# Kernel optimization log

Hardware: AMD Instinct MI355X
Metric: run time of the kernel (lower is better)

## Reference

```python
import jax, jax.numpy as jnp
import numpy as np
from jax import lax

NUM_CLUSTER = 128
N_ITERS = 10


def setup_inputs() -> dict:
    key = jax.random.key(0)
    feat_g = jax.random.normal(key, (131072, 256), dtype=jnp.float32)
    return {"feat_g": feat_g}


def _sq_dists(x, c):
    x2 = jnp.sum(x * x, axis=1, keepdims=True)            # [N,1]
    c2 = jnp.sum(c * c, axis=1)                           # [K]
    return x2 - 2.0 * (x @ c.T) + c2[None, :]


def _kmeans_fit(x, k, iters):
    n = x.shape[0]
    init_c = x[:k]  # deterministic init: first k points
    ones = jnp.ones((n,), dtype=x.dtype)

    def step(c, _):
        assign = jnp.argmin(_sq_dists(x, c), axis=1)                 # [N]
        sums = jax.ops.segment_sum(x, assign, num_segments=k)       # [K,d]
        counts = jax.ops.segment_sum(ones, assign, num_segments=k)  # [K]
        new_c = sums / jnp.maximum(counts, 1.0)[:, None]
        new_c = jnp.where(counts[:, None] > 0, new_c, c)  # keep empty clusters
        return new_c, None

    c, _ = lax.scan(step, init_c, None, length=iters)
    return c


def reference(feat_g):
    # view(batch, -1, dim) then view(-1, dim) is an identity reshape for the math
    x = lax.stop_gradient(feat_g)  # original detaches feat_gc before fit/predict
    c = _kmeans_fit(x, NUM_CLUSTER, N_ITERS)
    preds = jnp.argmin(_sq_dists(x, c), axis=1)  # [N] int labels
    return preds
```

## Files before the change

### kernel.cpp

```cpp
#include <hip/hip_runtime.h>

#define NPTS 131072
#define DIM 256
#define NK 128
#define NITER 10
#define SEG 16

typedef _Float16 half8 __attribute__((ext_vector_type(8)));
typedef _Float16 half4v __attribute__((ext_vector_type(4)));
typedef float f32x4 __attribute__((ext_vector_type(4)));

#define RSCALE 4096.0f
#define RINV 2.44140625e-4f

__global__ void x2_kernel(const float* __restrict__ x, float* __restrict__ x2) {
  int tid = threadIdx.x;
  int p = blockIdx.x * 16 + (tid >> 4);
  int part = tid & 15;
  const float4* xr = (const float4*)(x + (size_t)p * DIM);
  float s = 0.f;
#pragma unroll
  for (int j = 0; j < 4; ++j) {
    float4 v = xr[part * 4 + j];
    s += v.x * v.x;
    s += v.y * v.y;
    s += v.z * v.z;
    s += v.w * v.w;
  }
#pragma unroll
  for (int m = 8; m >= 1; m >>= 1) s += __shfl_xor(s, m, 16);
  if (part == 0) x2[p] = s;
}

__global__ void c2_kernel(const float* __restrict__ c, float* __restrict__ c2) {
  int k = blockIdx.x, lane = threadIdx.x;
  float4 v = ((const float4*)(c + (size_t)k * DIM))[lane];
  float s = v.x * v.x + v.y * v.y + v.z * v.z + v.w * v.w;
#pragma unroll
  for (int m = 32; m >= 1; m >>= 1) s += __shfl_xor(s, m, 64);
  if (lane == 0) c2[k] = s;
}

__global__ void convert_x_kernel(const float* __restrict__ x, _Float16* __restrict__ x1,
                                 _Float16* __restrict__ x2s) {
  int i = blockIdx.x * 256 + threadIdx.x;
  float4 v = ((const float4*)x)[i];
  float f[4] = {v.x, v.y, v.z, v.w};
  half4v h, l;
#pragma unroll
  for (int j = 0; j < 4; ++j) {
    _Float16 hi = (_Float16)f[j];
    float r = f[j] - (float)hi;
    h[j] = hi;
    l[j] = (_Float16)(r * RSCALE);
  }
  ((half4v*)x1)[i] = h;
  ((half4v*)x2s)[i] = l;
}

__global__ void convert_c_kernel(const float* __restrict__ c, _Float16* __restrict__ ct) {
  int i = blockIdx.x * 256 + threadIdx.x;
  int k = i >> 6;
  int d4 = i & 63;
  float4 v = ((const float4*)c)[i];
  float f[4] = {v.x, v.y, v.z, v.w};
  half4v h, l;
#pragma unroll
  for (int j = 0; j < 4; ++j) {
    _Float16 hi = (_Float16)f[j];
    float r = f[j] - (float)hi;
    h[j] = hi;
    l[j] = (_Float16)(r * RSCALE);
  }
  int ch = d4 >> 3;
  int idx4 = ch * 2048 + k * 8 + (d4 & 7);
  ((half4v*)ct)[idx4] = h;
  ((half4v*)ct)[idx4 + 1024] = l;
}

__global__ __launch_bounds__(256, 2) void assign_mfma_kernel(
    const _Float16* __restrict__ x1, const _Float16* __restrict__ x2s,
    const _Float16* __restrict__ ct, const float* __restrict__ x2,
    const float* __restrict__ c2, int* __restrict__ out) {
  __shared__ __align__(16) _Float16 cbuf[2][8192];

  int tid = threadIdx.x;
  int lane = tid & 63;
  int w = tid >> 6;
  int lcol = lane & 15;
  int lgrp = lane >> 4;
  int row0 = blockIdx.x * 128 + w * 32;

  const _Float16* xa = x1 + (size_t)(row0 + lcol) * DIM + lgrp * 8;
  const _Float16* xb = x2s + (size_t)(row0 + lcol) * DIM + lgrp * 8;
  const half8* ctv = (const half8*)ct;

  f32x4 acc1[2][8], acc2[2][8];
#pragma unroll
  for (int rt = 0; rt < 2; ++rt)
#pragma unroll
    for (int c8 = 0; c8 < 8; ++c8) {
      acc1[rt][c8] = f32x4{0.f, 0.f, 0.f, 0.f};
      acc2[rt][c8] = f32x4{0.f, 0.f, 0.f, 0.f};
    }

  half8 A1[2], A2[2], nA1[2], nA2[2], sreg[4];

#pragma unroll
  for (int r = 0; r < 4; ++r) sreg[r] = ctv[r * 256 + tid];
#pragma unroll
  for (int rt = 0; rt < 2; ++rt) {
    A1[rt] = *(const half8*)(xa + rt * 16 * DIM);
    A2[rt] = *(const half8*)(xb + rt * 16 * DIM);
  }
#pragma unroll
  for (int r = 0; r < 4; ++r) ((half8*)cbuf[0])[r * 256 + tid] = sreg[r];
  __syncthreads();

#pragma unroll
  for (int ck = 0; ck < 8; ++ck) {
    const int cb = ck & 1;
    if (ck < 7) {
#pragma unroll
      for (int r = 0; r < 4; ++r) sreg[r] = ctv[(ck + 1) * 1024 + r * 256 + tid];
#pragma unroll
      for (int rt = 0; rt < 2; ++rt) {
        nA1[rt] = *(const half8*)(xa + rt * 16 * DIM + (ck + 1) * 32);
        nA2[rt] = *(const half8*)(xb + rt * 16 * DIM + (ck + 1) * 32);
      }
    }
#pragma unroll
    for (int c8 = 0; c8 < 8; ++c8) {
      int bidx = (c8 * 16 + lcol) * 32 + lgrp * 8;
      half8 b1 = *(const half8*)&cbuf[cb][bidx];
      half8 b2 = *(const half8*)&cbuf[cb][4096 + bidx];
#pragma unroll
      for (int rt = 0; rt < 2; ++rt) {
        acc1[rt][c8] = __builtin_amdgcn_mfma_f32_16x16x32_f16(A1[rt], b1, acc1[rt][c8], 0, 0, 0);
        acc2[rt][c8] = __builtin_amdgcn_mfma_f32_16x16x32_f16(A1[rt], b2, acc2[rt][c8], 0, 0, 0);
        acc2[rt][c8] = __builtin_amdgcn_mfma_f32_16x16x32_f16(A2[rt], b1, acc2[rt][c8], 0, 0, 0);
      }
    }
    if (ck < 7) {
#pragma unroll
      for (int r = 0; r < 4; ++r) ((half8*)cbuf[cb ^ 1])[r * 256 + tid] = sreg[r];
#pragma unroll
      for (int rt = 0; rt < 2; ++rt) {
        A1[rt] = nA1[rt];
        A2[rt] = nA2[rt];
      }
      __syncthreads();
    }
  }

#pragma unroll
  for (int rt = 0; rt < 2; ++rt) {
    int pbase = row0 + rt * 16 + lgrp * 4;
    float x2p[4];
#pragma unroll
    for (int r = 0; r < 4; ++r) x2p[r] = x2[pbase + r];
    float bv[4];
    int bk[4];
#pragma unroll
    for (int r = 0; r < 4; ++r) { bv[r] = 3.4e38f; bk[r] = 0; }
#pragma unroll
    for (int c8 = 0; c8 < 8; ++c8) {
      int kc = c8 * 16 + lcol;
      float c2k = c2[kc];
#pragma unroll
      for (int r = 0; r < 4; ++r) {
        float dot = fmaf(acc2[rt][c8][r], RINV, acc1[rt][c8][r]);
        float d = fmaf(-2.f, dot, x2p[r]) + c2k;
        if (d < bv[r]) { bv[r] = d; bk[r] = kc; }
      }
    }
#pragma unroll
    for (int m = 1; m <= 8; m <<= 1) {
#pragma unroll
      for (int r = 0; r < 4; ++r) {
        float ov = __shfl_xor(bv[r], m, 64);
        int ok = __shfl_xor(bk[r], m, 64);
        if (ov < bv[r] || (ov == bv[r] && ok < bk[r])) { bv[r] = ov; bk[r] = ok; }
      }
    }
    if (lcol == 0) {
#pragma unroll
      for (int r = 0; r < 4; ++r) out[pbase + r] = bk[r];
    }
  }
}

__global__ void assign_kernel(const float* __restrict__ x, const float* __restrict__ c,
                              const float* __restrict__ x2, const float* __restrict__ c2,
                              int* __restrict__ assign_out) {
  __shared__ float4 xs4[64 * 4];
  __shared__ float4 cs4[128 * 4];
  __shared__ float redv[64][17];
  __shared__ int redk[64][17];

  int tid = threadIdx.x;
  int tx = tid & 15;
  int ty = tid >> 4;
  int row0 = blockIdx.x * 64;

  float acc[4][8];
#pragma unroll
  for (int a = 0; a < 4; ++a)
#pragma unroll
    for (int b = 0; b < 8; ++b) acc[a][b] = 0.f;

  for (int ck = 0; ck < 16; ++ck) {
    {
      int p = tid >> 2, d4 = tid & 3;
      float4 v = *(const float4*)(x + (size_t)(row0 + p) * DIM + ck * 16 + d4 * 4);
      xs4[p * 4 + (d4 ^ ((p >> 2) & 3))] = v;
    }
#pragma unroll
    for (int r = 0; r < 2; ++r) {
      int idx = tid + r * 256;
      int kk = idx >> 2, dd = idx & 3;
      float4 v = *(const float4*)(c + (size_t)kk * DIM + ck * 16 + dd * 4);
      cs4[kk * 4 + (dd ^ ((kk >> 3) & 3))] = v;
    }
    __syncthreads();
#pragma unroll
    for (int d4 = 0; d4 < 4; ++d4) {
      float4 xr[4], cr[8];
#pragma unroll
      for (int pp = 0; pp < 4; ++pp) xr[pp] = xs4[(tx * 4 + pp) * 4 + (d4 ^ (tx & 3))];
#pragma unroll
      for (int kk = 0; kk < 8; ++kk) cr[kk] = cs4[(ty * 8 + kk) * 4 + (d4 ^ (ty & 3))];
#pragma unroll
      for (int pp = 0; pp < 4; ++pp)
#pragma unroll
        for (int kk = 0; kk < 8; ++kk) {
          acc[pp][kk] = fmaf(xr[pp].x, cr[kk].x, acc[pp][kk]);
          acc[pp][kk] = fmaf(xr[pp].y, cr[kk].y, acc[pp][kk]);
          acc[pp][kk] = fmaf(xr[pp].z, cr[kk].z, acc[pp][kk]);
          acc[pp][kk] = fmaf(xr[pp].w, cr[kk].w, acc[pp][kk]);
        }
    }
    __syncthreads();
  }

  float x2p[4];
#pragma unroll
  for (int pp = 0; pp < 4; ++pp) x2p[pp] = x2[row0 + tx * 4 + pp];

  float bestv[4];
  int bestk[4];
#pragma unroll
  for (int pp = 0; pp < 4; ++pp) { bestv[pp] = 3.4e38f; bestk[pp] = 0; }
#pragma unroll
  for (int kk = 0; kk < 8; ++kk) {
    float c2k = c2[ty * 8 + kk];
#pragma unroll
    for (int pp = 0; pp < 4; ++pp) {
      float d = fmaf(-2.f, acc[pp][kk], x2p[pp]) + c2k;
      if (d < bestv[pp]) { bestv[pp] = d; bestk[pp] = ty * 8 + kk; }
    }
  }
#pragma unroll
  for (int pp = 0; pp < 4; ++pp) {
    redv[tx * 4 + pp][ty] = bestv[pp];
    redk[tx * 4 + pp][ty] = bestk[pp];
  }
  __syncthreads();
  if (tid < 64) {
    float bv = redv[tid][0];
    int bk = redk[tid][0];
#pragma unroll
    for (int t = 1; t < 16; ++t) {
      float v = redv[tid][t];
      if (v < bv) { bv = v; bk = redk[tid][t]; }
    }
    assign_out[row0 + tid] = bk;
  }
}

__global__ void hist_kernel(const int* __restrict__ assign_in, int* __restrict__ hist) {
  __shared__ int h[NK];
  int tid = threadIdx.x, b = blockIdx.x;
  if (tid < NK) h[tid] = 0;
  __syncthreads();
#pragma unroll
  for (int r = 0; r < 4; ++r) {
    int a = assign_in[b * 1024 + r * 256 + tid];
    atomicAdd(&h[a], 1);
  }
  __syncthreads();
  if (tid < NK) hist[b * NK + tid] = h[tid];
}

__global__ void scan_kernel(const int* __restrict__ hist, int* __restrict__ base,
                            int* __restrict__ counts, int* __restrict__ cbase) {
  __shared__ int h[128 * NK];
  int tid = threadIdx.x;
  for (int i = tid; i < 128 * NK; i += 256) h[i] = hist[i];
  __syncthreads();
  if (tid < NK) {
    int run = 0;
    for (int b = 0; b < 128; ++b) {
      int v = h[b * NK + tid];
      h[b * NK + tid] = run;
      run += v;
    }
    counts[tid] = run;
  }
  __syncthreads();
  if (tid == 0) {
    int cb = 0;
#pragma unroll 4
    for (int j = 0; j < NK; ++j) {
      cbase[j] = cb;
      cb += counts[j];
    }
  }
  __syncthreads();
  if (tid < NK) {
    int cbk = cbase[tid];
    for (int b = 0; b < 128; ++b) base[b * NK + tid] = h[b * NK + tid] + cbk;
  }
}

__global__ void scatter_kernel(const int* __restrict__ assign_in, const int* __restrict__ base,
                               int* __restrict__ perm) {
  __shared__ int cnt[NK];
  int lane = threadIdx.x, b = blockIdx.x;
  cnt[lane] = base[b * NK + lane];
  cnt[lane + 64] = base[b * NK + lane + 64];
  __syncthreads();
  for (int r = 0; r < 16; ++r) {
    int p = b * 1024 + r * 64 + lane;
    int a = assign_in[p];
    unsigned long long mask = ~0ull;
#pragma unroll
    for (int j = 0; j < 7; ++j) {
      unsigned long long bal = __ballot((a >> j) & 1);
      mask &= ((a >> j) & 1) ? bal : ~bal;
    }
    int rank = __popcll(mask & ((1ull << lane) - 1ull));
    int pos = cnt[a] + rank;
    perm[pos] = p;
    __syncthreads();
    if (rank == 0) cnt[a] += (int)__popcll(mask);
    __syncthreads();
  }
}

__global__ __launch_bounds__(256) void seg_sum_v2_kernel(
    const float* __restrict__ x, const int* __restrict__ perm,
    const int* __restrict__ counts, const int* __restrict__ cbase,
    float* __restrict__ partial) {
  __shared__ float4 red[4][64];
  int tid = threadIdx.x;
  int tg = tid >> 6;
  int lane = tid & 63;
  int k = blockIdx.x, s = blockIdx.y;
  int cnt = counts[k], off = cbase[k];
  int j0 = (int)(((long long)cnt * s) / SEG);
  int j1 = (int)(((long long)cnt * (s + 1)) / SEG);
  int len = j1 - j0;
  int jj0 = j0 + (int)(((long long)len * tg) / 4);
  int jj1 = j0 + (int)(((long long)len * (tg + 1)) / 4);

  float4 acc = {0.f, 0.f, 0.f, 0.f};
  int j = jj0;
  for (; j + 2 <= jj1; j += 2) {
    int p0 = perm[off + j];
    int p1 = perm[off + j + 1];
    float4 v0 = ((const float4*)(x + (size_t)p0 * DIM))[lane];
    float4 v1 = ((const float4*)(x + (size_t)p1 * DIM))[lane];
    acc.x += v0.x; acc.y += v0.y; acc.z += v0.z; acc.w += v0.w;
    acc.x += v1.x; acc.y += v1.y; acc.z += v1.z; acc.w += v1.w;
  }
  for (; j < jj1; ++j) {
    int p = perm[off + j];
    float4 v = ((const float4*)(x + (size_t)p * DIM))[lane];
    acc.x += v.x; acc.y += v.y; acc.z += v.z; acc.w += v.w;
  }
  red[tg][lane] = acc;
  __syncthreads();
  if (tg == 0) {
    float4 s0 = red[0][lane], s1 = red[1][lane], s2 = red[2][lane], s3 = red[3][lane];
    float4 t;
    t.x = ((s0.x + s1.x) + s2.x) + s3.x;
    t.y = ((s0.y + s1.y) + s2.y) + s3.y;
    t.z = ((s0.z + s1.z) + s2.z) + s3.z;
    t.w = ((s0.w + s1.w) + s2.w) + s3.w;
    ((float4*)(partial + ((size_t)k * SEG + s) * DIM))[lane] = t;
  }
}

__global__ void seg_sum_kernel(const float* __restrict__ x, const int* __restrict__ perm,
                               const int* __restrict__ counts, const int* __restrict__ cbase,
                               float* __restrict__ partial) {
  int k = blockIdx.x, s = blockIdx.y, d = threadIdx.x;
  int cnt = counts[k], off = cbase[k];
  int j0 = (int)(((long long)cnt * s) / SEG);
  int j1 = (int)(((long long)cnt * (s + 1)) / SEG);
  float sum = 0.f;
  int j = j0;
  for (; j + 4 <= j1; j += 4) {
    int p0 = perm[off + j + 0];
    int p1 = perm[off + j + 1];
    int p2 = perm[off + j + 2];
    int p3 = perm[off + j + 3];
    sum += x[(size_t)p0 * DIM + d];
    sum += x[(size_t)p1 * DIM + d];
    sum += x[(size_t)p2 * DIM + d];
    sum += x[(size_t)p3 * DIM + d];
  }
  for (; j < j1; ++j) sum += x[(size_t)perm[off + j] * DIM + d];
  partial[((size_t)k * SEG + s) * DIM + d] = sum;
}

__global__ void reduce_kernel(const float* __restrict__ partial, const int* __restrict__ counts,
                              float* __restrict__ c, float* __restrict__ c2) {
  __shared__ float wsum[4];
  int k = blockIdx.x, d = threadIdx.x;
  int cnt = counts[k];
  float s = 0.f;
#pragma unroll
  for (int t = 0; t < SEG; ++t) s += partial[((size_t)k * SEG + t) * DIM + d];

  float nc;
  if (cnt > 0)
    nc = s / fmaxf((float)cnt, 1.0f);
  else
    nc = c[(size_t)k * DIM + d];
  c[(size_t)k * DIM + d] = nc;

  float s2 = nc * nc;
#pragma unroll
  for (int m = 32; m >= 1; m >>= 1) s2 += __shfl_xor(s2, m, 64);
  if ((threadIdx.x & 63) == 0) wsum[threadIdx.x >> 6] = s2;
  __syncthreads();
  if (threadIdx.x == 0) c2[k] = wsum[0] + wsum[1] + wsum[2] + wsum[3];
}

extern "C" void kernel_launch(void* const* d_in, const int* in_sizes, int n_in,
                              void* d_out, int out_size, void* d_ws, size_t ws_size,
                              hipStream_t stream) {
  const float* x = (const float*)d_in[0];
  char* ws = (char*)d_ws;

  const size_t NEED_BIG = 138282496;
  bool use_mfma = ws_size >= NEED_BIG;

  if (use_mfma) {
    _Float16* x1 = (_Float16*)(ws + 0);
    _Float16* x2s = (_Float16*)(ws + 67108864);
    float* c = (float*)(ws + 134217728);
    _Float16* ct = (_Float16*)(ws + 134348800);
    float* c2 = (float*)(ws + 134479872);
    float* x2 = (float*)(ws + 134480384);
    int* assignb = (int*)(ws + 135004672);
    int* hist = (int*)(ws + 135528960);
    int* base = (int*)(ws + 135594496);
    int* counts = (int*)(ws + 135660032);
    int* cbase = (int*)(ws + 135660544);
    int* perm = (int*)(ws + 135661056);
    float* partial = (float*)(ws + 136185344);

    hipMemcpyAsync(c, x, (size_t)NK * DIM * sizeof(float), hipMemcpyDeviceToDevice, stream);
    convert_x_kernel<<<NPTS * DIM / 4 / 256, 256, 0, stream>>>(x, x1, x2s);
    x2_kernel<<<NPTS / 16, 256, 0, stream>>>(x, x2);
    c2_kernel<<<NK, 64, 0, stream>>>(c, c2);
    convert_c_kernel<<<NK * DIM / 4 / 256, 256, 0, stream>>>(c, ct);

    for (int it = 0; it < NITER; ++it) {
      assign_mfma_kernel<<<NPTS / 128, 256, 0, stream>>>(x1, x2s, ct, x2, c2, assignb);
      hist_kernel<<<NPTS / 1024, 256, 0, stream>>>(assignb, hist);
      scan_kernel<<<1, 256, 0, stream>>>(hist, base, counts, cbase);
      scatter_kernel<<<NPTS / 1024, 64, 0, stream>>>(assignb, base, perm);
      seg_sum_v2_kernel<<<dim3(NK, SEG), 256, 0, stream>>>(x, perm, counts, cbase, partial);
      reduce_kernel<<<NK, 256, 0, stream>>>(partial, counts, c, c2);
      convert_c_kernel<<<NK * DIM / 4 / 256, 256, 0, stream>>>(c, ct);
    }
    assign_mfma_kernel<<<NPTS / 128, 256, 0, stream>>>(x1, x2s, ct, x2, c2, (int*)d_out);
  } else {
    float* c = (float*)(ws + 0);
    float* c2 = (float*)(ws + 131072);
    float* x2 = (float*)(ws + 132096);
    int* assignb = (int*)(ws + 656384);
    int* hist = (int*)(ws + 1180672);
    int* base = (int*)(ws + 1246208);
    int* counts = (int*)(ws + 1311744);
    int* cbase = (int*)(ws + 1312256);
    int* perm = (int*)(ws + 1312768);
    float* partial = (float*)(ws + 1837056);

    hipMemcpyAsync(c, x, (size_t)NK * DIM * sizeof(float), hipMemcpyDeviceToDevice, stream);
    x2_kernel<<<NPTS / 16, 256, 0, stream>>>(x, x2);
    c2_kernel<<<NK, 64, 0, stream>>>(c, c2);

    for (int it = 0; it < NITER; ++it) {
      assign_kernel<<<NPTS / 64, 256, 0, stream>>>(x, c, x2, c2, assignb);
      hist_kernel<<<NPTS / 1024, 256, 0, stream>>>(assignb, hist);
      scan_kernel<<<1, 256, 0, stream>>>(hist, base, counts, cbase);
      scatter_kernel<<<NPTS / 1024, 64, 0, stream>>>(assignb, base, perm);
      seg_sum_kernel<<<dim3(NK, SEG), 256, 0, stream>>>(x, perm, counts, cbase, partial);
      reduce_kernel<<<NK, 256, 0, stream>>>(partial, counts, c, c2);
    }
    assign_kernel<<<NPTS / 64, 256, 0, stream>>>(x, c, x2, c2, (int*)d_out);
  }
}
```

Measured before the change: 1.063 ms.

## Fuse histogram into assign, balance segment sums, fuse centroid conversion into reduce

```diff
diff --git a/kernel.cpp b/kernel.cpp
--- a/kernel.cpp
+++ b/kernel.cpp
@@ -5,6 +5,8 @@
 #define NK 128
 #define NITER 10
 #define SEG 16
+#define TILE 128
+#define MAXSEGS (NPTS / TILE + NK)
 
 typedef _Float16 half8 __attribute__((ext_vector_type(8)));
 typedef _Float16 half4v __attribute__((ext_vector_type(4)));
@@ -78,11 +80,13 @@
   ((half4v*)ct)[idx4 + 1024] = l;
 }
 
+template <bool DOHIST>
 __global__ __launch_bounds__(256, 2) void assign_mfma_kernel(
     const _Float16* __restrict__ x1, const _Float16* __restrict__ x2s,
     const _Float16* __restrict__ ct, const float* __restrict__ x2,
-    const float* __restrict__ c2, int* __restrict__ out) {
+    const float* __restrict__ c2, int* __restrict__ out, int* __restrict__ hist) {
   __shared__ __align__(16) _Float16 cbuf[2][8192];
+  __shared__ int hcnt[NK];
 
   int tid = threadIdx.x;
   int lane = tid & 63;
@@ -91,6 +95,8 @@
   int lgrp = lane >> 4;
   int row0 = blockIdx.x * 128 + w * 32;
 
+  if (DOHIST && tid < NK) hcnt[tid] = 0;
+
   const _Float16* xa = x1 + (size_t)(row0 + lcol) * DIM + lgrp * 8;
   const _Float16* xb = x2s + (size_t)(row0 + lcol) * DIM + lgrp * 8;
   const half8* ctv = (const half8*)ct;
@@ -185,7 +191,18 @@
     }
     if (lcol == 0) {
 #pragma unroll
-      for (int r = 0; r < 4; ++r) out[pbase + r] = bk[r];
+      for (int r = 0; r < 4; ++r) {
+        out[pbase + r] = bk[r];
+        if (DOHIST) atomicAdd(&hcnt[bk[r]], 1);
+      }
+    }
+  }
+
+  if (DOHIST) {
+    __syncthreads();
+    if (tid < NK) {
+      int v = hcnt[tid];
+      if (v) atomicAdd(&hist[(blockIdx.x >> 3) * NK + tid], v);
     }
   }
 }
@@ -292,12 +309,17 @@
   if (tid < NK) hist[b * NK + tid] = h[tid];
 }
 
-__global__ void scan_kernel(const int* __restrict__ hist, int* __restrict__ base,
-                            int* __restrict__ counts, int* __restrict__ cbase) {
+__global__ void scan_kernel(int* __restrict__ hist, int* __restrict__ base,
+                            int* __restrict__ counts, int* __restrict__ cbase,
+                            int* __restrict__ segbase) {
   __shared__ int h[128 * NK];
+  __shared__ int scnt[NK];
+  __shared__ int scb[NK];
+  __shared__ int ssb[NK + 1];
   int tid = threadIdx.x;
   for (int i = tid; i < 128 * NK; i += 256) h[i] = hist[i];
   __syncthreads();
+  for (int i = tid; i < 128 * NK; i += 256) hist[i] = 0;
   if (tid < NK) {
     int run = 0;
     for (int b = 0; b < 128; ++b) {
@@ -305,22 +327,27 @@
       h[b * NK + tid] = run;
       run += v;
     }
+    scnt[tid] = run;
     counts[tid] = run;
   }
   __syncthreads();
   if (tid == 0) {
-    int cb = 0;
-#pragma unroll 4
+    int cb = 0, sb = 0;
     for (int j = 0; j < NK; ++j) {
-      cbase[j] = cb;
-      cb += counts[j];
-    }
+      scb[j] = cb;
+      cb += scnt[j];
+      ssb[j] = sb;
+      sb += (scnt[j] + TILE - 1) / TILE;
+    }
+    ssb[NK] = sb;
   }
   __syncthreads();
   if (tid < NK) {
-    int cbk = cbase[tid];
+    cbase[tid] = scb[tid];
+    int cbk = scb[tid];
     for (int b = 0; b < 128; ++b) base[b * NK + tid] = h[b * NK + tid] + cbk;
   }
+  if (tid <= NK) segbase[tid] = ssb[tid];
 }
 
 __global__ void scatter_kernel(const int* __restrict__ assign_in, const int* __restrict__ base,
@@ -329,7 +356,6 @@
   int lane = threadIdx.x, b = blockIdx.x;
   cnt[lane] = base[b * NK + lane];
   cnt[lane + 64] = base[b * NK + lane + 64];
-  __syncthreads();
   for (int r = 0; r < 16; ++r) {
     int p = b * 1024 + r * 64 + lane;
     int a = assign_in[p];
@@ -342,42 +368,51 @@
     int rank = __popcll(mask & ((1ull << lane) - 1ull));
     int pos = cnt[a] + rank;
     perm[pos] = p;
-    __syncthreads();
     if (rank == 0) cnt[a] += (int)__popcll(mask);
-    __syncthreads();
-  }
-}
-
-__global__ __launch_bounds__(256) void seg_sum_v2_kernel(
+  }
+}
+
+__global__ __launch_bounds__(256) void seg_sum_v3_kernel(
     const float* __restrict__ x, const int* __restrict__ perm,
     const int* __restrict__ counts, const int* __restrict__ cbase,
-    float* __restrict__ partial) {
+    const int* __restrict__ segbase, float* __restrict__ partial) {
+  __shared__ int sb[NK + 1];
   __shared__ float4 red[4][64];
   int tid = threadIdx.x;
+  if (tid <= NK) sb[tid] = segbase[tid];
+  __syncthreads();
+  int b = blockIdx.x;
+  if (b >= sb[NK]) return;
+  int lo = 0, hi = NK - 1;
+  while (lo < hi) {
+    int mid = (lo + hi + 1) >> 1;
+    if (sb[mid] <= b) lo = mid;
+    else hi = mid - 1;
+  }
+  int k = lo;
+  int cnt = counts[k], off = cbase[k];
+  int j0 = (b - sb[k]) * TILE;
+  int j1 = min(j0 + TILE, cnt);
+
   int tg = tid >> 6;
   int lane = tid & 63;
-  int k = blockIdx.x, s = blockIdx.y;
-  int cnt = counts[k], off = cbase[k];
-  int j0 = (int)(((long long)cnt * s) / SEG);
-  int j1 = (int)(((long long)cnt * (s + 1)) / SEG);
   int len = j1 - j0;
-  int jj0 = j0 + (int)(((long long)len * tg) / 4);
-  int jj1 = j0 + (int)(((long long)len * (tg + 1)) / 4);
+  int jj0 = j0 + (len * tg) / 4;
+  int jj1 = j0 + (len * (tg + 1)) / 4;
+  int n = jj1 - jj0;
+
+  int pv = 0;
+  if (lane < n) pv = perm[off + jj0 + lane];
 
   float4 acc = {0.f, 0.f, 0.f, 0.f};
-  int j = jj0;
-  for (; j + 2 <= jj1; j += 2) {
-    int p0 = perm[off + j];
-    int p1 = perm[off + j + 1];
-    float4 v0 = ((const float4*)(x + (size_t)p0 * DIM))[lane];
-    float4 v1 = ((const float4*)(x + (size_t)p1 * DIM))[lane];
-    acc.x += v0.x; acc.y += v0.y; acc.z += v0.z; acc.w += v0.w;
-    acc.x += v1.x; acc.y += v1.y; acc.z += v1.z; acc.w += v1.w;
-  }
-  for (; j < jj1; ++j) {
-    int p = perm[off + j];
+#pragma unroll 4
+  for (int j = 0; j < n; ++j) {
+    int p = __shfl(pv, j, 64);
     float4 v = ((const float4*)(x + (size_t)p * DIM))[lane];
-    acc.x += v.x; acc.y += v.y; acc.z += v.z; acc.w += v.w;
+    acc.x += v.x;
+    acc.y += v.y;
+    acc.z += v.z;
+    acc.w += v.w;
   }
   red[tg][lane] = acc;
   __syncthreads();
@@ -388,8 +423,50 @@
     t.y = ((s0.y + s1.y) + s2.y) + s3.y;
     t.z = ((s0.z + s1.z) + s2.z) + s3.z;
     t.w = ((s0.w + s1.w) + s2.w) + s3.w;
-    ((float4*)(partial + ((size_t)k * SEG + s) * DIM))[lane] = t;
-  }
+    ((float4*)(partial + (size_t)b * DIM))[lane] = t;
+  }
+}
+
+__global__ void reduce_kernel(const float* __restrict__ partial, const int* __restrict__ counts,
+                              const int* __restrict__ segbase, float* __restrict__ c,
+                              float* __restrict__ c2, _Float16* __restrict__ ct) {
+  __shared__ float wsum[4];
+  int k = blockIdx.x, d = threadIdx.x;
+  int cnt = counts[k];
+  int s0 = segbase[k], s1 = segbase[k + 1];
+  float s = 0.f;
+  int t = s0;
+  for (; t + 4 <= s1; t += 4) {
+    float p0 = partial[(size_t)(t + 0) * DIM + d];
+    float p1 = partial[(size_t)(t + 1) * DIM + d];
+    float p2 = partial[(size_t)(t + 2) * DIM + d];
+    float p3 = partial[(size_t)(t + 3) * DIM + d];
+    s += ((p0 + p1) + p2) + p3;
+  }
+  for (; t < s1; ++t) s += partial[(size_t)t * DIM + d];
+
+  float nc;
+  if (cnt > 0)
+    nc = s / fmaxf((float)cnt, 1.0f);
+  else
+    nc = c[(size_t)k * DIM + d];
+  c[(size_t)k * DIM + d] = nc;
+
+  {
+    _Float16 hi = (_Float16)nc;
+    float r = nc - (float)hi;
+    _Float16 lov = (_Float16)(r * RSCALE);
+    int ch = d >> 5, dd = d & 31;
+    ct[ch * 8192 + k * 32 + dd] = hi;
+    ct[ch * 8192 + k * 32 + dd + 4096] = lov;
+  }
+
+  float s2 = nc * nc;
+#pragma unroll
+  for (int m = 32; m >= 1; m >>= 1) s2 += __shfl_xor(s2, m, 64);
+  if ((threadIdx.x & 63) == 0) wsum[threadIdx.x >> 6] = s2;
+  __syncthreads();
+  if (threadIdx.x == 0) c2[k] = wsum[0] + wsum[1] + wsum[2] + wsum[3];
 }
 
 __global__ void seg_sum_kernel(const float* __restrict__ x, const int* __restrict__ perm,
@@ -415,28 +492,56 @@
   partial[((size_t)k * SEG + s) * DIM + d] = sum;
 }
 
-__global__ void reduce_kernel(const float* __restrict__ partial, const int* __restrict__ counts,
-                              float* __restrict__ c, float* __restrict__ c2) {
+__global__ void reduce_fb_kernel(const float* __restrict__ partial, const int* __restrict__ counts,
+                                 float* __restrict__ c, float* __restrict__ c2) {
   __shared__ float wsum[4];
   int k = blockIdx.x, d = threadIdx.x;
   int cnt = counts[k];
   float s = 0.f;
 #pragma unroll
   for (int t = 0; t < SEG; ++t) s += partial[((size_t)k * SEG + t) * DIM + d];
-
   float nc;
   if (cnt > 0)
     nc = s / fmaxf((float)cnt, 1.0f);
   else
     nc = c[(size_t)k * DIM + d];
   c[(size_t)k * DIM + d] = nc;
-
   float s2 = nc * nc;
 #pragma unroll
   for (int m = 32; m >= 1; m >>= 1) s2 += __shfl_xor(s2, m, 64);
   if ((threadIdx.x & 63) == 0) wsum[threadIdx.x >> 6] = s2;
   __syncthreads();
   if (threadIdx.x == 0) c2[k] = wsum[0] + wsum[1] + wsum[2] + wsum[3];
+}
+
+__global__ void scan_fb_kernel(const int* __restrict__ hist, int* __restrict__ base,
+                               int* __restrict__ counts, int* __restrict__ cbase) {
+  __shared__ int h[128 * NK];
+  int tid = threadIdx.x;
+  for (int i = tid; i < 128 * NK; i += 256) h[i] = hist[i];
+  __syncthreads();
+  if (tid < NK) {
+    int run = 0;
+    for (int b = 0; b < 128; ++b) {
+      int v = h[b * NK + tid];
+      h[b * NK + tid] = run;
+      run += v;
+    }
+    counts[tid] = run;
+  }
+  __syncthreads();
+  if (tid == 0) {
+    int cb = 0;
+    for (int j = 0; j < NK; ++j) {
+      cbase[j] = cb;
+      cb += counts[j];
+    }
+  }
+  __syncthreads();
+  if (tid < NK) {
+    int cbk = cbase[tid];
+    for (int b = 0; b < 128; ++b) base[b * NK + tid] = h[b * NK + tid] + cbk;
+  }
 }
 
 extern "C" void kernel_launch(void* const* d_in, const int* in_sizes, int n_in,
@@ -445,7 +550,7 @@
   const float* x = (const float*)d_in[0];
   char* ws = (char*)d_ws;
 
-  const size_t NEED_BIG = 138282496;
+  const size_t NEED_BIG = 138283520;
   bool use_mfma = ws_size >= NEED_BIG;
 
   if (use_mfma) {
@@ -462,23 +567,24 @@
     int* cbase = (int*)(ws + 135660544);
     int* perm = (int*)(ws + 135661056);
     float* partial = (float*)(ws + 136185344);
+    int* segbase = (int*)(ws + 138282496);
 
     hipMemcpyAsync(c, x, (size_t)NK * DIM * sizeof(float), hipMemcpyDeviceToDevice, stream);
+    hipMemsetAsync(hist, 0, 128 * NK * sizeof(int), stream);
     convert_x_kernel<<<NPTS * DIM / 4 / 256, 256, 0, stream>>>(x, x1, x2s);
     x2_kernel<<<NPTS / 16, 256, 0, stream>>>(x, x2);
     c2_kernel<<<NK, 64, 0, stream>>>(c, c2);
     convert_c_kernel<<<NK * DIM / 4 / 256, 256, 0, stream>>>(c, ct);
 
     for (int it = 0; it < NITER; ++it) {
-      assign_mfma_kernel<<<NPTS / 128, 256, 0, stream>>>(x1, x2s, ct, x2, c2, assignb);
-      hist_kernel<<<NPTS / 1024, 256, 0, stream>>>(assignb, hist);
-      scan_kernel<<<1, 256, 0, stream>>>(hist, base, counts, cbase);
+      assign_mfma_kernel<true><<<NPTS / 128, 256, 0, stream>>>(x1, x2s, ct, x2, c2, assignb, hist);
+      scan_kernel<<<1, 256, 0, stream>>>(hist, base, counts, cbase, segbase);
       scatter_kernel<<<NPTS / 1024, 64, 0, stream>>>(assignb, base, perm);
-      seg_sum_v2_kernel<<<dim3(NK, SEG), 256, 0, stream>>>(x, perm, counts, cbase, partial);
-      reduce_kernel<<<NK, 256, 0, stream>>>(partial, counts, c, c2);
-      convert_c_kernel<<<NK * DIM / 4 / 256, 256, 0, stream>>>(c, ct);
-    }
-    assign_mfma_kernel<<<NPTS / 128, 256, 0, stream>>>(x1, x2s, ct, x2, c2, (int*)d_out);
+      seg_sum_v3_kernel<<<MAXSEGS, 256, 0, stream>>>(x, perm, counts, cbase, segbase, partial);
+      reduce_kernel<<<NK, 256, 0, stream>>>(partial, counts, segbase, c, c2, ct);
+    }
+    assign_mfma_kernel<false><<<NPTS / 128, 256, 0, stream>>>(x1, x2s, ct, x2, c2, (int*)d_out,
+                                                              hist);
   } else {
     float* c = (float*)(ws + 0);
     float* c2 = (float*)(ws + 131072);
@@ -498,10 +604,10 @@
     for (int it = 0; it < NITER; ++it) {
       assign_kernel<<<NPTS / 64, 256, 0, stream>>>(x, c, x2, c2, assignb);
       hist_kernel<<<NPTS / 1024, 256, 0, stream>>>(assignb, hist);
-      scan_kernel<<<1, 256, 0, stream>>>(hist, base, counts, cbase);
+      scan_fb_kernel<<<1, 256, 0, stream>>>(hist, base, counts, cbase);
       scatter_kernel<<<NPTS / 1024, 64, 0, stream>>>(assignb, base, perm);
       seg_sum_kernel<<<dim3(NK, SEG), 256, 0, stream>>>(x, perm, counts, cbase, partial);
-      reduce_kernel<<<NK, 256, 0, stream>>>(partial, counts, c, c2);
+      reduce_fb_kernel<<<NK, 256, 0, stream>>>(partial, counts, c, c2);
     }
     assign_kernel<<<NPTS / 64, 256, 0, stream>>>(x, c, x2, c2, (int*)d_out);
   }
```

Measured after the change: 1.029 ms. 1.03x faster.
